# Performance work log

Measured on AMD Instinct MI355X. Metric: run time of the kernel, lower is better.

The kernel has to match this reference:

```python
import jax, jax.numpy as jnp
import numpy as np

K = 20  # neighbors


def knn_idx(x, k):
    # x: [B, C, N]; returns indices of k nearest neighbors (incl. self): [B, N, k]
    xx = jnp.sum(x * x, axis=1)                          # [B, N]
    inner = jnp.einsum('bcn,bcm->bnm', x, x)             # [B, N, N]
    pd = 2.0 * inner - xx[:, :, None] - xx[:, None, :]   # -squared distance
    _, idx = jax.lax.top_k(pd, k)                        # [B, N, k]
    return idx


def graph_feature(x, k):
    # x: [B, C, N] -> edge features [B, 2C, N, k]
    idx = knn_idx(x, k)                                  # [B, N, k]
    xt = jnp.swapaxes(x, 1, 2)                           # [B, N, C]
    nbr = jax.vmap(lambda f, i: f[i])(xt, idx)           # [B, N, k, C]
    ctr = xt[:, :, None, :]                              # [B, N, 1, C]
    feat = jnp.concatenate(
        [nbr - ctr, jnp.broadcast_to(ctr, nbr.shape)], axis=-1)  # [B, N, k, 2C]
    return jnp.transpose(feat, (0, 3, 1, 2))             # [B, 2C, N, k]


def blk2(x, w, s, t):
    # 1x1 Conv2d (no bias) + folded BN + LeakyReLU(0.2); x: [B, C, N, k]
    y = jnp.einsum('oc,bcnk->bonk', w, x)
    y = y * s[None, :, None, None] + t[None, :, None, None]
    return jax.nn.leaky_relu(y, 0.2)


def blk1(x, w, s, t):
    # 1x1 Conv1d (no bias) + folded BN + LeakyReLU(0.2); x: [B, C, N]
    y = jnp.einsum('oc,bcn->bon', w, x)
    y = y * s[None, :, None] + t[None, :, None]
    return jax.nn.leaky_relu(y, 0.2)


def setup_inputs() -> dict:
    key = jax.random.key(0)
    ks = jax.random.split(key, 32)
    inp = {'x': jax.random.normal(ks[0], (16, 2, 2048), jnp.float32)}
    wdims = [(64, 4), (64, 64), (64, 128), (64, 64), (64, 128),
             (1024, 192), (512, 1216), (256, 512), (1, 256)]
    for i, (o, c) in enumerate(wdims):
        inp[f'w{i+1}'] = jax.random.normal(ks[1 + i], (o, c), jnp.float32) * np.float32((2.0 / c) ** 0.5)
    bdims = [64, 64, 64, 64, 64, 1024, 512, 256]
    for i, d in enumerate(bdims):
        inp[f's{i+1}'] = jax.random.uniform(ks[10 + i], (d,), jnp.float32, 0.5, 1.5)
        inp[f't{i+1}'] = jax.random.normal(ks[18 + i], (d,), jnp.float32) * 0.1
    return inp


def reference(x, w1, w2, w3, w4, w5, w6, w7, w8, w9,
              s1, s2, s3, s4, s5, s6, s7, s8,
              t1, t2, t3, t4, t5, t6, t7, t8):
    B, _, N = x.shape
    h = graph_feature(x, K)                 # [B, 4, N, k]
    h = blk2(h, w1, s1, t1)
    h = blk2(h, w2, s2, t2)
    x1 = jnp.max(h, axis=-1)                # [B, 64, N]
    h = graph_feature(x1, K)                # [B, 128, N, k]
    h = blk2(h, w3, s3, t3)
    h = blk2(h, w4, s4, t4)
    x2 = jnp.max(h, axis=-1)                # [B, 64, N]
    h = graph_feature(x2, K)                # [B, 128, N, k]
    h = blk2(h, w5, s5, t5)
    x3 = jnp.max(h, axis=-1)                # [B, 64, N]
    cat = jnp.concatenate([x1, x2, x3], axis=1)   # [B, 192, N]
    e = blk1(cat, w6, s6, t6)               # [B, 1024, N]
    g = jnp.max(e, axis=-1, keepdims=True)  # global max [B, 1024, 1]
    g = jnp.broadcast_to(g, (B, g.shape[1], N))
    h = jnp.concatenate([g, x1, x2, x3], axis=1)  # [B, 1216, N]
    h = blk1(h, w7, s7, t7)
    h = blk1(h, w8, s8, t8)                 # dropout = identity (eval)
    y = jnp.einsum('oc,bcn->bon', w9, h)    # [B, 1, N]
    return jax.nn.sigmoid(y.reshape(B, -1))
```

## Files before the change

kernel.cpp:

```cpp
#include <hip/hip_runtime.h>
#include <math.h>

#define KNNK 20
#define BEFORE(v1, g1, v2, g2) (((v1) > (v2)) || ((v1) == (v2) && (g1) < (g2)))

typedef unsigned short u16;
typedef unsigned int u32;
typedef unsigned long long u64;
typedef __attribute__((ext_vector_type(8))) short short8v;
typedef __attribute__((ext_vector_type(4))) float f32x4;

__device__ __forceinline__ float lrelu(float v) { return v >= 0.f ? v : 0.2f * v; }

__device__ __forceinline__ u16 f2bf(float v) {
    u32 u = __float_as_uint(v);
    u += 0x7fffu + ((u >> 16) & 1u);
    return (u16)(u >> 16);
}
__device__ __forceinline__ float bf2f(u16 h) { return __uint_as_float(((u32)h) << 16); }

__device__ __forceinline__ u32 ordf(float v) {
    u32 u = __float_as_uint(v);
    return u ^ ((u32)((int)u >> 31) | 0x80000000u);
}
__device__ __forceinline__ u64 mkkey(float v, int g) {
    return ((u64)ordf(v) << 32) | (u32)(~(u32)g);
}

__device__ __forceinline__ void cvt8(const float* __restrict__ p, short8v& H8, short8v& M8, short8v& L8) {
    float4 a = *(const float4*)(p);
    float4 b4 = *(const float4*)(p + 4);
    float v[8] = {a.x, a.y, a.z, a.w, b4.x, b4.y, b4.z, b4.w};
    short8v H, M, L;
#pragma unroll
    for (int i = 0; i < 8; ++i) {
        float x = v[i];
        u16 h = f2bf(x);
        float r1 = x - bf2f(h);
        u16 m = f2bf(r1);
        float r2 = r1 - bf2f(m);
        H[i] = (short)h;
        M[i] = (short)m;
        L[i] = (short)f2bf(r2);
    }
    H8 = H; M8 = M; L8 = L;
}

__global__ __launch_bounds__(256) void xx_kernel(const float* __restrict__ f, long bstride, int C,
                                                 float* __restrict__ xx) {
    int i = blockIdx.x * 256 + threadIdx.x;
    int b = i >> 11, n = i & 2047;
    const float* fb = f + (long)b * bstride;
    float s = 0.f;
    for (int c = 0; c < C; ++c) { float v = fb[c * 2048 + n]; s = fmaf(v, v, s); }
    xx[i] = s;
}

__device__ __forceinline__ void topk_row(const float* __restrict__ srow, int lane, int* __restrict__ orow) {
    float b1 = -INFINITY, b2 = -INFINITY, b3 = -INFINITY;
    int j1 = 0, j2 = 0, j3 = 0;
#pragma unroll
    for (int j = 0; j < 32; ++j) {
        float vv = srow[lane + 64 * j];
        bool c1 = vv > b1;
        bool c2 = vv > b2;
        bool c3 = vv > b3;
        b3 = c2 ? b2 : (c3 ? vv : b3);
        j3 = c2 ? j2 : (c3 ? j : j3);
        b2 = c1 ? b1 : (c2 ? vv : b2);
        j2 = c1 ? j1 : (c2 ? j : j2);
        b1 = c1 ? vv : b1;
        j1 = c1 ? j : j1;
    }
    u64 ka = mkkey(b1, lane + (j1 << 6));
#pragma unroll
    for (int size = 2; size <= 64; size <<= 1) {
#pragma unroll
        for (int stride = size >> 1; stride >= 1; stride >>= 1) {
            u64 ok = __shfl_xor(ka, stride);
            bool low = (lane & stride) == 0;
            bool asc = (lane & size) == 0;
            bool f = ka > ok;
            bool take = (low == asc) ? f : !f;
            ka = take ? ka : ok;
        }
    }
    u64 w19 = __shfl(ka, 19);
    unsigned used = (1u << j1) | (1u << j2) | (1u << j3);
    u64 pend = mkkey(b2, lane + (j2 << 6));
    int pstate = 0;
    while (__any(pend > w19)) {
        u64 act = __ballot(pend > w19);
        int L = __ffsll((long long)act) - 1;
        u64 ck = __shfl(pend, L);
        u64 cfb = __ballot(lane < 20 && ck > ka);
        int p = 20 - __popcll(cfb);
        u64 up = __shfl_up(ka, 1);
        if (lane < 20) {
            if (lane > p) ka = up;
            else if (lane == p) ka = ck;
        }
        if (lane == L) {
            if (pstate == 0) {
                pend = mkkey(b3, lane + (j3 << 6));
                pstate = 1;
            } else {
                float nb = -INFINITY;
                int nj = 0;
#pragma unroll
                for (int j = 0; j < 32; ++j) {
                    float vvv = ((used >> j) & 1u) ? -INFINITY : srow[lane + 64 * j];
                    if (vvv > nb) { nb = vvv; nj = j; }
                }
                used |= 1u << nj;
                pend = mkkey(nb, lane + (nj << 6));
            }
        }
        w19 = __shfl(ka, 19);
    }
    if (lane < KNNK) orow[lane] = (int)(~(u32)ka) & 2047;
}

__device__ __forceinline__ u64 topk20_half(const float* __restrict__ srow, int lane, int colbase) {
    float b1 = -INFINITY, b2 = -INFINITY, b3 = -INFINITY;
    int j1 = 0, j2 = 0, j3 = 0;
#pragma unroll
    for (int j = 0; j < 16; ++j) {
        float vv = srow[lane + 64 * j];
        bool c1 = vv > b1;
        bool c2 = vv > b2;
        bool c3 = vv > b3;
        b3 = c2 ? b2 : (c3 ? vv : b3);
        j3 = c2 ? j2 : (c3 ? j : j3);
        b2 = c1 ? b1 : (c2 ? vv : b2);
        j2 = c1 ? j1 : (c2 ? j : j2);
        b1 = c1 ? vv : b1;
        j1 = c1 ? j : j1;
    }
    u64 ka = mkkey(b1, colbase + lane + (j1 << 6));
#pragma unroll
    for (int size = 2; size <= 64; size <<= 1) {
#pragma unroll
        for (int stride = size >> 1; stride >= 1; stride >>= 1) {
            u64 ok = __shfl_xor(ka, stride);
            bool low = (lane & stride) == 0;
            bool asc = (lane & size) == 0;
            bool f = ka > ok;
            bool take = (low == asc) ? f : !f;
            ka = take ? ka : ok;
        }
    }
    u64 w19 = __shfl(ka, 19);
    unsigned used = (1u << j1) | (1u << j2) | (1u << j3);
    u64 pend = mkkey(b2, colbase + lane + (j2 << 6));
    int pstate = 0;
    while (__any(pend > w19)) {
        u64 act = __ballot(pend > w19);
        int L = __ffsll((long long)act) - 1;
        u64 ck = __shfl(pend, L);
        u64 cfb = __ballot(lane < 20 && ck > ka);
        int p = 20 - __popcll(cfb);
        u64 up = __shfl_up(ka, 1);
        if (lane < 20) {
            if (lane > p) ka = up;
            else if (lane == p) ka = ck;
        }
        if (lane == L) {
            if (pstate == 0) {
                pend = mkkey(b3, colbase + lane + (j3 << 6));
                pstate = 1;
            } else {
                float nb = -INFINITY;
                int nj = 0;
#pragma unroll
                for (int j = 0; j < 16; ++j) {
                    float vvv = ((used >> j) & 1u) ? -INFINITY : srow[lane + 64 * j];
                    if (vvv > nb) { nb = vvv; nj = j; }
                }
                used |= 1u << nj;
                pend = mkkey(nb, colbase + lane + (nj << 6));
            }
        }
        w19 = __shfl(ka, 19);
    }
    return ka;
}

__device__ __forceinline__ u64 merge20(u64 kA, u64 kB, int lane) {
    u64 kb = __shfl(kB, (lane - 20) & 63);
    u64 ka = lane < 20 ? kA : (lane < 40 ? kb : 0ULL);
#pragma unroll
    for (int size = 2; size <= 64; size <<= 1) {
#pragma unroll
        for (int stride = size >> 1; stride >= 1; stride >>= 1) {
            u64 ok = __shfl_xor(ka, stride);
            bool low = (lane & stride) == 0;
            bool asc = (lane & size) == 0;
            bool f = ka > ok;
            bool take = (low == asc) ? f : !f;
            ka = take ? ka : ok;
        }
    }
    return ka;
}

__global__ __launch_bounds__(512, 4) void knn_kernel(const float* __restrict__ f, long bstride, int C,
                                                     const float* __restrict__ xx, int* __restrict__ idx_out) {
    __shared__ __align__(16) float pd[8 * 2048];
    __shared__ __align__(16) float Asm[16 * 64];
    int b = blockIdx.y;
    int n0 = blockIdx.x * 16;
    int t = threadIdx.x;
    const float* fb = f + (long)b * bstride;

    for (int e = t; e < C * 16; e += 512) {
        int c = e >> 4, j = e & 15;
        Asm[e] = fb[c * 2048 + n0 + j];
    }
    __syncthreads();

    float acc[16][4];
#pragma unroll
    for (int i = 0; i < 16; ++i)
#pragma unroll
        for (int j = 0; j < 4; ++j) acc[i][j] = 0.f;
    int m0 = t * 4;
    for (int c = 0; c < C; ++c) {
        float4 b4 = *(const float4*)(fb + c * 2048 + m0);
        float bv[4] = {b4.x, b4.y, b4.z, b4.w};
        const float* ar = Asm + c * 16;
        float4 a0 = *(const float4*)(ar);
        float4 a1 = *(const float4*)(ar + 4);
        float4 a2 = *(const float4*)(ar + 8);
        float4 a3 = *(const float4*)(ar + 12);
        float av[16] = {a0.x, a0.y, a0.z, a0.w, a1.x, a1.y, a1.z, a1.w,
                        a2.x, a2.y, a2.z, a2.w, a3.x, a3.y, a3.z, a3.w};
#pragma unroll
        for (int i = 0; i < 16; ++i)
#pragma unroll
            for (int j = 0; j < 4; ++j) acc[i][j] = fmaf(av[i], bv[j], acc[i][j]);
    }
    float4 xm4 = *(const float4*)(xx + b * 2048 + m0);
    float xm[4] = {xm4.x, xm4.y, xm4.z, xm4.w};

    int wave = t >> 6, lane = t & 63;

    {
        float4 xa0 = *(const float4*)(xx + b * 2048 + n0);
        float4 xa1 = *(const float4*)(xx + b * 2048 + n0 + 4);
        float xn[8] = {xa0.x, xa0.y, xa0.z, xa0.w, xa1.x, xa1.y, xa1.z, xa1.w};
#pragma unroll
        for (int i = 0; i < 8; ++i) {
            float4 o;
            o.x = (2.f * acc[i][0] - xn[i]) - xm[0];
            o.y = (2.f * acc[i][1] - xn[i]) - xm[1];
            o.z = (2.f * acc[i][2] - xn[i]) - xm[2];
            o.w = (2.f * acc[i][3] - xn[i]) - xm[3];
            *(float4*)(pd + i * 2048 + m0) = o;
        }
    }
    __syncthreads();
    topk_row(pd + wave * 2048, lane, idx_out + ((long)b * 2048 + n0 + wave) * KNNK);
    __syncthreads();

    {
        float4 xb0 = *(const float4*)(xx + b * 2048 + n0 + 8);
        float4 xb1 = *(const float4*)(xx + b * 2048 + n0 + 12);
        float xn[8] = {xb0.x, xb0.y, xb0.z, xb0.w, xb1.x, xb1.y, xb1.z, xb1.w};
#pragma unroll
        for (int i = 0; i < 8; ++i) {
            float4 o;
            o.x = (2.f * acc[8 + i][0] - xn[i]) - xm[0];
            o.y = (2.f * acc[8 + i][1] - xn[i]) - xm[1];
            o.z = (2.f * acc[8 + i][2] - xn[i]) - xm[2];
            o.w = (2.f * acc[8 + i][3] - xn[i]) - xm[3];
            *(float4*)(pd + i * 2048 + m0) = o;
        }
    }
    __syncthreads();
    topk_row(pd + wave * 2048, lane, idx_out + ((long)b * 2048 + n0 + 8 + wave) * KNNK);
}

__global__ __launch_bounds__(256) void split3t_kernel(const float* __restrict__ src, long bstride,
                                                      u16* __restrict__ oh, u16* __restrict__ om,
                                                      u16* __restrict__ ol) {
    __shared__ float lds[32][65];
    int b = blockIdx.y;
    int kt = blockIdx.x & 1, nt = blockIdx.x >> 1;
    int k0 = kt * 32, n0 = nt * 64, t = threadIdx.x;
#pragma unroll
    for (int i = 0; i < 8; ++i) {
        int e = t + i * 256;
        int k = e >> 6, n = e & 63;
        lds[k][n] = src[(long)b * bstride + (long)(k0 + k) * 2048 + n0 + n];
    }
    __syncthreads();
    int n = t >> 2, kq = t & 3;
    u16 hv[8], mv[8], lv[8];
#pragma unroll
    for (int i = 0; i < 8; ++i) {
        float v = lds[kq * 8 + i][n];
        u16 h = f2bf(v);
        float r1 = v - bf2f(h);
        u16 m = f2bf(r1);
        float r2 = r1 - bf2f(m);
        hv[i] = h; mv[i] = m; lv[i] = f2bf(r2);
    }
    long off = ((long)b * 2048 + n0 + n) * 64 + k0 + kq * 8;
    uint4 uh, um, ul;
    uh.x = (u32)hv[0] | ((u32)hv[1] << 16); uh.y = (u32)hv[2] | ((u32)hv[3] << 16);
    uh.z = (u32)hv[4] | ((u32)hv[5] << 16); uh.w = (u32)hv[6] | ((u32)hv[7] << 16);
    um.x = (u32)mv[0] | ((u32)mv[1] << 16); um.y = (u32)mv[2] | ((u32)mv[3] << 16);
    um.z = (u32)mv[4] | ((u32)mv[5] << 16); um.w = (u32)mv[6] | ((u32)mv[7] << 16);
    ul.x = (u32)lv[0] | ((u32)lv[1] << 16); ul.y = (u32)lv[2] | ((u32)lv[3] << 16);
    ul.z = (u32)lv[4] | ((u32)lv[5] << 16); ul.w = (u32)lv[6] | ((u32)lv[7] << 16);
    *(uint4*)(oh + off) = uh;
    *(uint4*)(om + off) = um;
    *(uint4*)(ol + off) = ul;
}

__global__ __launch_bounds__(512, 4) void knn_mfma_kernel(const u16* __restrict__ Sh, const u16* __restrict__ Sm,
                                                          const u16* __restrict__ Sl, const float* __restrict__ xx,
                                                          int* __restrict__ idx_out) {
    __shared__ __align__(16) float pd[16 * 1028];
    int b = blockIdx.y, n0 = blockIdx.x * 16, t = threadIdx.x;
    int wave = t >> 6, lane = t & 63, l15 = lane & 15, lq = lane >> 4;
    const u16* bh_ = Sh + (long)b * 2048 * 64;
    const u16* bm_ = Sm + (long)b * 2048 * 64;
    const u16* bl_ = Sl + (long)b * 2048 * 64;

    long ab = (long)(n0 + l15) * 64 + lq * 8;
    short8v ah0 = *(const short8v*)(bh_ + ab), ah1 = *(const short8v*)(bh_ + ab + 32);
    short8v am0 = *(const short8v*)(bm_ + ab), am1 = *(const short8v*)(bm_ + ab + 32);
    short8v al0 = *(const short8v*)(bl_ + ab), al1 = *(const short8v*)(bl_ + ab + 32);
    float4 xn4 = *(const float4*)(xx + b * 2048 + n0 + lq * 4);
    float xn[4] = {xn4.x, xn4.y, xn4.z, xn4.w};

    u64 kA0 = 0, kA1 = 0, kB0 = 0, kB1 = 0;
#pragma unroll
    for (int half = 0; half < 2; ++half) {
        int jb = half * 1024 + wave * 128;
        short8v Bh0[2], Bh1[2], Bm0[2], Bm1[2], Bl0[2], Bl1[2];
        {
            long bb = (long)(jb + l15) * 64 + lq * 8;
            Bh0[0] = *(const short8v*)(bh_ + bb); Bh1[0] = *(const short8v*)(bh_ + bb + 32);
            Bm0[0] = *(const short8v*)(bm_ + bb); Bm1[0] = *(const short8v*)(bm_ + bb + 32);
            Bl0[0] = *(const short8v*)(bl_ + bb); Bl1[0] = *(const short8v*)(bl_ + bb + 32);
        }
#pragma unroll
        for (int tt = 0; tt < 8; ++tt) {
            const int cur = tt & 1, nxt = cur ^ 1;
            if (tt < 7) {
                long bb = (long)(jb + (tt + 1) * 16 + l15) * 64 + lq * 8;
                Bh0[nxt] = *(const short8v*)(bh_ + bb); Bh1[nxt] = *(const short8v*)(bh_ + bb + 32);
                Bm0[nxt] = *(const short8v*)(bm_ + bb); Bm1[nxt] = *(const short8v*)(bm_ + bb + 32);
                Bl0[nxt] = *(const short8v*)(bl_ + bb); Bl1[nxt] = *(const short8v*)(bl_ + bb + 32);
            }
            f32x4 p = {0.f, 0.f, 0.f, 0.f}, q = {0.f, 0.f, 0.f, 0.f};
            p = __builtin_amdgcn_mfma_f32_16x16x32_bf16(ah0, Bh0[cur], p, 0, 0, 0);
            q = __builtin_amdgcn_mfma_f32_16x16x32_bf16(ah0, Bm0[cur], q, 0, 0, 0);
            p = __builtin_amdgcn_mfma_f32_16x16x32_bf16(am0, Bh0[cur], p, 0, 0, 0);
            q = __builtin_amdgcn_mfma_f32_16x16x32_bf16(am0, Bm0[cur], q, 0, 0, 0);
            p = __builtin_amdgcn_mfma_f32_16x16x32_bf16(ah0, Bl0[cur], p, 0, 0, 0);
            q = __builtin_amdgcn_mfma_f32_16x16x32_bf16(al0, Bh0[cur], q, 0, 0, 0);
            p = __builtin_amdgcn_mfma_f32_16x16x32_bf16(ah1, Bh1[cur], p, 0, 0, 0);
            q = __builtin_amdgcn_mfma_f32_16x16x32_bf16(ah1, Bm1[cur], q, 0, 0, 0);
            p = __builtin_amdgcn_mfma_f32_16x16x32_bf16(am1, Bh1[cur], p, 0, 0, 0);
            q = __builtin_amdgcn_mfma_f32_16x16x32_bf16(am1, Bm1[cur], q, 0, 0, 0);
            p = __builtin_amdgcn_mfma_f32_16x16x32_bf16(ah1, Bl1[cur], p, 0, 0, 0);
            q = __builtin_amdgcn_mfma_f32_16x16x32_bf16(al1, Bh1[cur], q, 0, 0, 0);
            int col = jb + tt * 16 + l15;
            float xmc = xx[(long)b * 2048 + col];
            f32x4 r = p + q;
            int lcol = col - half * 1024;
            pd[(lq * 4 + 0) * 1028 + lcol] = (2.f * r[0] - xn[0]) - xmc;
            pd[(lq * 4 + 1) * 1028 + lcol] = (2.f * r[1] - xn[1]) - xmc;
            pd[(lq * 4 + 2) * 1028 + lcol] = (2.f * r[2] - xn[2]) - xmc;
            pd[(lq * 4 + 3) * 1028 + lcol] = (2.f * r[3] - xn[3]) - xmc;
        }
        __syncthreads();
        if (half == 0) {
            kA0 = topk20_half(pd + (2 * wave) * 1028, lane, 0);
            kA1 = topk20_half(pd + (2 * wave + 1) * 1028, lane, 0);
            __syncthreads();
        } else {
            kB0 = topk20_half(pd + (2 * wave) * 1028, lane, 1024);
            kB1 = topk20_half(pd + (2 * wave + 1) * 1028, lane, 1024);
        }
    }
    u64 f0 = merge20(kA0, kB0, lane);
    u64 f1 = merge20(kA1, kB1, lane);
    if (lane < KNNK) {
        idx_out[((long)b * 2048 + n0 + 2 * wave) * KNNK + lane] = (int)(~(u32)f0) & 2047;
        idx_out[((long)b * 2048 + n0 + 2 * wave + 1) * KNNK + lane] = (int)(~(u32)f1) & 2047;
    }
}

__global__ __launch_bounds__(256) void pq_kernel(const float* __restrict__ f, long bstride, int C,
                                                 const float* __restrict__ W, float* __restrict__ P,
                                                 float* __restrict__ Q) {
    __shared__ __align__(16) float wa[64 * 64];
    __shared__ __align__(16) float wq[64 * 64];
    __shared__ __align__(16) float X[64 * 64];
    int b = blockIdx.y, n0 = blockIdx.x * 64, t = threadIdx.x;
    const float* fb = f + (long)b * bstride;
    for (int e = t; e < C * 64; e += 256) {
        int k = e >> 6, c = e & 63;
        float a = W[c * 2 * C + k];
        float bv = W[c * 2 * C + C + k];
        wa[k * 64 + c] = a;
        wq[k * 64 + c] = bv - a;
    }
    for (int e = t; e < C * 64; e += 256) {
        int k = e >> 6, j = e & 63;
        X[e] = fb[k * 2048 + n0 + j];
    }
    __syncthreads();
    int cg = t >> 4, ng = t & 15;
    float accP[4][4] = {}, accQ[4][4] = {};
    for (int k = 0; k < C; ++k) {
        float4 a4 = *(const float4*)(wa + k * 64 + cg * 4);
        float4 q4 = *(const float4*)(wq + k * 64 + cg * 4);
        float4 x4 = *(const float4*)(X + k * 64 + ng * 4);
        float av[4] = {a4.x, a4.y, a4.z, a4.w};
        float qv[4] = {q4.x, q4.y, q4.z, q4.w};
        float xv[4] = {x4.x, x4.y, x4.z, x4.w};
#pragma unroll
        for (int i = 0; i < 4; ++i)
#pragma unroll
            for (int j = 0; j < 4; ++j) {
                accP[i][j] = fmaf(av[i], xv[j], accP[i][j]);
                accQ[i][j] = fmaf(qv[i], xv[j], accQ[i][j]);
            }
    }
#pragma unroll
    for (int j = 0; j < 4; ++j) {
        long n = n0 + ng * 4 + j;
        float4 pv = {accP[0][j], accP[1][j], accP[2][j], accP[3][j]};
        float4 qv = {accQ[0][j], accQ[1][j], accQ[2][j], accQ[3][j]};
        *(float4*)(P + ((long)b * 2048 + n) * 64 + cg * 4) = pv;
        *(float4*)(Q + ((long)b * 2048 + n) * 64 + cg * 4) = qv;
    }
}

__global__ __launch_bounds__(256) void splitw3_kernel(const float* __restrict__ W, u16* __restrict__ h,
                                                      u16* __restrict__ m, u16* __restrict__ l) {
    int i = blockIdx.x * 256 + threadIdx.x;
    float v = W[i];
    u16 hh = f2bf(v);
    float r1 = v - bf2f(hh);
    u16 mm = f2bf(r1);
    float r2 = r1 - bf2f(mm);
    h[i] = hh;
    m[i] = mm;
    l[i] = f2bf(r2);
}

__global__ __launch_bounds__(256) void edge2_mfma_kernel(
    const float* __restrict__ P, const float* __restrict__ Q, const int* __restrict__ idx,
    const u16* __restrict__ Wh, const u16* __restrict__ Wm, const u16* __restrict__ Wl,
    const float* __restrict__ sa, const float* __restrict__ ta, const float* __restrict__ sb,
    const float* __restrict__ tb, float* __restrict__ out, int cofs) {
    __shared__ __align__(16) float h1t[192 * 68];
    __shared__ int idxl[160];
    int b = blockIdx.y, n0 = blockIdx.x * 8, t = threadIdx.x;
    if (t < 160) idxl[t] = idx[((long)b * 2048 + n0) * KNNK + t];
    __syncthreads();

    for (int it = t; it < 2560; it += 256) {
        int col = it % 160, cg = it / 160;
        int p = col / 20;
        int j = idxl[col];
        int n = n0 + p;
        float4 pv = *(const float4*)(P + ((long)b * 2048 + j) * 64 + cg * 4);
        float4 qv = *(const float4*)(Q + ((long)b * 2048 + n) * 64 + cg * 4);
        float4 sv = *(const float4*)(sa + cg * 4);
        float4 tv = *(const float4*)(ta + cg * 4);
        float4 o;
        o.x = lrelu(fmaf(sv.x, pv.x + qv.x, tv.x));
        o.y = lrelu(fmaf(sv.y, pv.y + qv.y, tv.y));
        o.z = lrelu(fmaf(sv.z, pv.z + qv.z, tv.z));
        o.w = lrelu(fmaf(sv.w, pv.w + qv.w, tv.w));
        *(float4*)(h1t + col * 68 + cg * 4) = o;
    }
    for (int it = t; it < 512; it += 256) {
        int col = 160 + (it & 31), cg = it >> 5;
        float4 z = {0.f, 0.f, 0.f, 0.f};
        *(float4*)(h1t + col * 68 + cg * 4) = z;
    }
    __syncthreads();

    int wave = t >> 6, lane = t & 63, l15 = lane & 15, lq = lane >> 4;
    f32x4 acc[3][4];
#pragma unroll
    for (int ct = 0; ct < 3; ++ct)
#pragma unroll
        for (int mt = 0; mt < 4; ++mt) {
            f32x4 z = {0.f, 0.f, 0.f, 0.f};
            acc[ct][mt] = z;
        }

#pragma unroll
    for (int ct = 0; ct < 3; ++ct) {
        int col = (wave * 3 + ct) * 16 + l15;
        short8v bh[2], bm[2], bl[2];
#pragma unroll
        for (int kh = 0; kh < 2; ++kh) cvt8(h1t + col * 68 + kh * 32 + lq * 8, bh[kh], bm[kh], bl[kh]);
#pragma unroll
        for (int mt = 0; mt < 4; ++mt) {
#pragma unroll
            for (int kh = 0; kh < 2; ++kh) {
                int wo = (mt * 16 + l15) * 64 + kh * 32 + lq * 8;
                short8v ah = *(const short8v*)(Wh + wo);
                short8v am = *(const short8v*)(Wm + wo);
                short8v al = *(const short8v*)(Wl + wo);
                acc[ct][mt] = __builtin_amdgcn_mfma_f32_16x16x32_bf16(ah, bh[kh], acc[ct][mt], 0, 0, 0);
                acc[ct][mt] = __builtin_amdgcn_mfma_f32_16x16x32_bf16(ah, bm[kh], acc[ct][mt], 0, 0, 0);
                acc[ct][mt] = __builtin_amdgcn_mfma_f32_16x16x32_bf16(am, bh[kh], acc[ct][mt], 0, 0, 0);
                acc[ct][mt] = __builtin_amdgcn_mfma_f32_16x16x32_bf16(am, bm[kh], acc[ct][mt], 0, 0, 0);
                acc[ct][mt] = __builtin_amdgcn_mfma_f32_16x16x32_bf16(ah, bl[kh], acc[ct][mt], 0, 0, 0);
                acc[ct][mt] = __builtin_amdgcn_mfma_f32_16x16x32_bf16(al, bh[kh], acc[ct][mt], 0, 0, 0);
            }
        }
    }
    __syncthreads();

#pragma unroll
    for (int ct = 0; ct < 3; ++ct) {
        int col = (wave * 3 + ct) * 16 + l15;
#pragma unroll
        for (int mt = 0; mt < 4; ++mt) {
            float4 d = {acc[ct][mt][0], acc[ct][mt][1], acc[ct][mt][2], acc[ct][mt][3]};
            *(float4*)(h1t + col * 68 + mt * 16 + lq * 4) = d;
        }
    }
    __syncthreads();

    for (int id = t; id < 512; id += 256) {
        int co = id & 63, p = id >> 6;
        float sv = sb[co], tv = tb[co];
        float m = -INFINITY;
#pragma unroll 4
        for (int kk = 0; kk < KNNK; ++kk)
            m = fmaxf(m, lrelu(fmaf(sv, h1t[(p * 20 + kk) * 68 + co], tv)));
        out[(long)b * (192 * 2048) + (long)(cofs + co) * 2048 + n0 + p] = m;
    }
}

__global__ __launch_bounds__(256) void edge2_kernel(
    const float* __restrict__ P, const float* __restrict__ Q, const int* __restrict__ idx,
    const float* __restrict__ W2, const float* __restrict__ sa, const float* __restrict__ ta,
    const float* __restrict__ sb, const float* __restrict__ tb, float* __restrict__ out, int cofs) {
    __shared__ __align__(16) float h1[64 * 164];
    __shared__ __align__(16) float w2l[64 * 64];
    __shared__ int idxl[160];
    int b = blockIdx.y, n0 = blockIdx.x * 8, t = threadIdx.x;
    if (t < 160) idxl[t] = idx[((long)b * 2048 + n0) * KNNK + t];
    for (int e = t; e < 4096; e += 256) { int co = e >> 6, ci = e & 63; w2l[ci * 64 + co] = W2[e]; }
    __syncthreads();
    for (int it = t; it < 2560; it += 256) {
        int col = it % 160, cg = it / 160;
        int p = col / 20;
        int j = idxl[col];
        int n = n0 + p;
        float4 pv = *(const float4*)(P + ((long)b * 2048 + j) * 64 + cg * 4);
        float4 qv = *(const float4*)(Q + ((long)b * 2048 + n) * 64 + cg * 4);
        float4 sv = *(const float4*)(sa + cg * 4);
        float4 tv = *(const float4*)(ta + cg * 4);
        h1[(cg * 4 + 0) * 164 + col] = lrelu(fmaf(sv.x, pv.x + qv.x, tv.x));
        h1[(cg * 4 + 1) * 164 + col] = lrelu(fmaf(sv.y, pv.y + qv.y, tv.y));
        h1[(cg * 4 + 2) * 164 + col] = lrelu(fmaf(sv.z, pv.z + qv.z, tv.z));
        h1[(cg * 4 + 3) * 164 + col] = lrelu(fmaf(sv.w, pv.w + qv.w, tv.w));
    }
    __syncthreads();
    int p = t & 7, co2 = t >> 3, c0 = co2 * 2;
    float acc0[20], acc1[20];
#pragma unroll
    for (int q = 0; q < 20; ++q) { acc0[q] = 0.f; acc1[q] = 0.f; }
#pragma unroll 4
    for (int k = 0; k < 64; ++k) {
        float2 w = *(const float2*)(w2l + k * 64 + c0);
        const float* hr = h1 + k * 164 + p * 20;
#pragma unroll
        for (int q = 0; q < 5; ++q) {
            float4 h4 = *(const float4*)(hr + q * 4);
            acc0[q * 4 + 0] = fmaf(w.x, h4.x, acc0[q * 4 + 0]);
            acc0[q * 4 + 1] = fmaf(w.x, h4.y, acc0[q * 4 + 1]);
            acc0[q * 4 + 2] = fmaf(w.x, h4.z, acc0[q * 4 + 2]);
            acc0[q * 4 + 3] = fmaf(w.x, h4.w, acc0[q * 4 + 3]);
            acc1[q * 4 + 0] = fmaf(w.y, h4.x, acc1[q * 4 + 0]);
            acc1[q * 4 + 1] = fmaf(w.y, h4.y, acc1[q * 4 + 1]);
            acc1[q * 4 + 2] = fmaf(w.y, h4.z, acc1[q * 4 + 2]);
            acc1[q * 4 + 3] = fmaf(w.y, h4.w, acc1[q * 4 + 3]);
        }
    }
    float s0 = sb[c0], t0v = tb[c0], s1 = sb[c0 + 1], t1v = tb[c0 + 1];
    float m0 = -INFINITY, m1 = -INFINITY;
#pragma unroll
    for (int q = 0; q < 20; ++q) {
        m0 = fmaxf(m0, lrelu(fmaf(s0, acc0[q], t0v)));
        m1 = fmaxf(m1, lrelu(fmaf(s1, acc1[q], t1v)));
    }
    out[(long)b * (192 * 2048) + (long)(cofs + c0) * 2048 + n0 + p] = m0;
    out[(long)b * (192 * 2048) + (long)(cofs + c0 + 1) * 2048 + n0 + p] = m1;
}

__global__ __launch_bounds__(256) void edge1_kernel(const float* __restrict__ P, const float* __restrict__ Q,
                                                    const int* __restrict__ idx, const float* __restrict__ s,
                                                    const float* __restrict__ tt, float* __restrict__ out,
                                                    int cofs) {
    __shared__ int idxl[80];
    int b = blockIdx.y, n0 = blockIdx.x * 4, t = threadIdx.x;
    int c = t & 63, p = t >> 6;
    if (t < 80) idxl[t] = idx[((long)b * 2048 + n0) * KNNK + t];
    __syncthreads();
    float qv = Q[((long)b * 2048 + n0 + p) * 64 + c];
    float sc = s[c], tc = tt[c];
    float m = -INFINITY;
    for (int kk = 0; kk < KNNK; ++kk) {
        int j = idxl[p * KNNK + kk];
        float v = P[((long)b * 2048 + j) * 64 + c];
        m = fmaxf(m, lrelu(fmaf(sc, v + qv, tc)));
    }
    out[(long)b * (192 * 2048) + (long)(cofs + c) * 2048 + n0 + p] = m;
}

__global__ __launch_bounds__(256) void gemm_kernel(
    const float* __restrict__ W, int ldw, int Kdim, const float* __restrict__ X, long xbstride,
    const float* __restrict__ s, const float* __restrict__ tvec, const float* __restrict__ bias, int M,
    float* __restrict__ out, long obstride, float* __restrict__ maxout) {
    __shared__ __align__(16) float wl[32 * 68];
    __shared__ __align__(16) float xl[32 * 132];
    int b = blockIdx.z, ct = blockIdx.x * 64, nt = blockIdx.y * 128, t = threadIdx.x;
    const float* Xb = X + (long)b * xbstride;
    int cg = t >> 4, ng = t & 15;
    float acc[4][8];
#pragma unroll
    for (int i = 0; i < 4; ++i)
#pragma unroll
        for (int j = 0; j < 8; ++j) acc[i][j] = 0.f;
    for (int k0 = 0; k0 < Kdim; k0 += 32) {
        __syncthreads();
        for (int e = t; e < 2048; e += 256) {
            int c = e >> 5, k = e & 31;
            wl[k * 68 + c] = W[(long)(ct + c) * ldw + k0 + k];
        }
        for (int e = t; e < 4096; e += 256) {
            int k = e >> 7, j = e & 127;
            xl[k * 132 + j] = Xb[(long)(k0 + k) * 2048 + nt + j];
        }
        __syncthreads();
#pragma unroll 8
        for (int k = 0; k < 32; ++k) {
            float4 w4 = *(const float4*)(wl + k * 68 + cg * 4);
            float4 xa = *(const float4*)(xl + k * 132 + ng * 4);
            float4 xb = *(const float4*)(xl + k * 132 + 64 + ng * 4);
            float wv[4] = {w4.x, w4.y, w4.z, w4.w};
            float xv[8] = {xa.x, xa.y, xa.z, xa.w, xb.x, xb.y, xb.z, xb.w};
#pragma unroll
            for (int i = 0; i < 4; ++i)
#pragma unroll
                for (int j = 0; j < 8; ++j) acc[i][j] = fmaf(wv[i], xv[j], acc[i][j]);
        }
    }
    if (maxout) {
        __syncthreads();
        float* scr = xl;
#pragma unroll
        for (int i = 0; i < 4; ++i) {
            int c = ct + cg * 4 + i;
            float sv = s[c], tv = tvec[c];
            float m = -INFINITY;
#pragma unroll
            for (int j = 0; j < 8; ++j) m = fmaxf(m, lrelu(fmaf(sv, acc[i][j], tv)));
            scr[(cg * 4 + i) * 16 + ng] = m;
        }
        __syncthreads();
        if (t < 64) {
            float m = scr[t * 16];
            for (int j = 1; j < 16; ++j) m = fmaxf(m, scr[t * 16 + j]);
            maxout[((long)b * M + ct + t) * 16 + blockIdx.y] = m;
        }
    } else {
#pragma unroll
        for (int i = 0; i < 4; ++i) {
            int c = ct + cg * 4 + i;
            float bv = bias ? bias[b * M + c] : 0.f;
            float sv = s[c], tv = tvec[c];
            float4 o0, o1;
            o0.x = lrelu(fmaf(sv, acc[i][0] + bv, tv));
            o0.y = lrelu(fmaf(sv, acc[i][1] + bv, tv));
            o0.z = lrelu(fmaf(sv, acc[i][2] + bv, tv));
            o0.w = lrelu(fmaf(sv, acc[i][3] + bv, tv));
            o1.x = lrelu(fmaf(sv, acc[i][4] + bv, tv));
            o1.y = lrelu(fmaf(sv, acc[i][5] + bv, tv));
            o1.z = lrelu(fmaf(sv, acc[i][6] + bv, tv));
            o1.w = lrelu(fmaf(sv, acc[i][7] + bv, tv));
            float* op = out + (long)b * obstride + (long)c * 2048 + nt + ng * 4;
            *(float4*)op = o0;
            *(float4*)(op + 64) = o1;
        }
    }
}

__global__ __launch_bounds__(256) void splitw_kernel(const float* __restrict__ W, int ldw, int koff, int K,
                                                     long total, u16* __restrict__ hi, u16* __restrict__ lo) {
    long i = (long)blockIdx.x * 256 + threadIdx.x;
    if (i >= total) return;
    long m = i / K, k = i - m * K;
    float v = W[m * ldw + koff + k];
    u16 h = f2bf(v);
    hi[i] = h;
    lo[i] = f2bf(v - bf2f(h));
}

__global__ __launch_bounds__(256) void splitx_kernel(const float* __restrict__ cat, u16* __restrict__ hi,
                                                     u16* __restrict__ lo) {
    __shared__ float lds[32][65];
    int b = blockIdx.y;
    int kt = blockIdx.x % 6, nt = blockIdx.x / 6;
    int k0 = kt * 32, n0 = nt * 64;
    int t = threadIdx.x;
#pragma unroll
    for (int i = 0; i < 8; ++i) {
        int e = t + i * 256;
        int k = e >> 6, n = e & 63;
        lds[k][n] = cat[(long)b * (192 * 2048) + (long)(k0 + k) * 2048 + n0 + n];
    }
    __syncthreads();
    int n = t >> 2, kq = t & 3;
    u16 hv[8], lv[8];
#pragma unroll
    for (int i = 0; i < 8; ++i) {
        float v = lds[kq * 8 + i][n];
        u16 h = f2bf(v);
        hv[i] = h;
        lv[i] = f2bf(v - bf2f(h));
    }
    long off = ((long)b * 2048 + n0 + n) * 192 + k0 + kq * 8;
    uint4 uh, ul;
    uh.x = (u32)hv[0] | ((u32)hv[1] << 16); uh.y = (u32)hv[2] | ((u32)hv[3] << 16);
    uh.z = (u32)hv[4] | ((u32)hv[5] << 16); uh.w = (u32)hv[6] | ((u32)hv[7] << 16);
    ul.x = (u32)lv[0] | ((u32)lv[1] << 16); ul.y = (u32)lv[2] | ((u32)lv[3] << 16);
    ul.z = (u32)lv[4] | ((u32)lv[5] << 16); ul.w = (u32)lv[6] | ((u32)lv[7] << 16);
    *(uint4*)(hi + off) = uh;
    *(uint4*)(lo + off) = ul;
}

template <int MT, int NT, bool MAXOUT>
__global__ __launch_bounds__(256, 2) void gemm_mfma(
    const u16* __restrict__ Whi, const u16* __restrict__ Wlo, const u16* __restrict__ Xhi,
    const u16* __restrict__ Xlo, int K, int M, const float* __restrict__ s,
    const float* __restrict__ tvec, const float* __restrict__ bias, float* __restrict__ outf,
    long obstride, u16* __restrict__ ohi, u16* __restrict__ olo, int oK, float* __restrict__ maxout) {
    constexpr int BM = MT * 32, BN = NT * 32;
    __shared__ __align__(16) u16 Ah[BM * 32], Al[BM * 32], Bh[BN * 32], Bl[BN * 32];
    __shared__ float scr[MAXOUT ? BM * 2 : 1];

    int b = blockIdx.z;
    int m0 = blockIdx.x * BM;
    int n0 = blockIdx.y * BN;
    int t = threadIdx.x;
    int wave = t >> 6, lane = t & 63;
    int wm = (wave >> 1) * (MT * 16);
    int wn = (wave & 1) * (NT * 16);
    const int l15 = lane & 15, lq = lane >> 4;
    const int kcs = lq ^ ((l15 >> 1) & 3);

    const u16* Xbh = Xhi + (long)b * 2048 * K;
    const u16* Xbl = Xlo + (long)b * 2048 * K;

    f32x4 zero4 = {0.f, 0.f, 0.f, 0.f};
    f32x4 acc[MT][NT];
#pragma unroll
    for (int i = 0; i < MT; ++i)
#pragma unroll
        for (int j = 0; j < NT; ++j) acc[i][j] = zero4;

    for (int k0 = 0; k0 < K; k0 += 32) {
        __syncthreads();
#pragma unroll
        for (int u = t; u < BM * 4; u += 256) {
            int row = u >> 2, kc = (u & 3) ^ ((row >> 1) & 3);
            long ga = (long)(m0 + row) * K + k0 + kc * 8;
            *(uint4*)(Ah + u * 8) = *(const uint4*)(Whi + ga);
            *(uint4*)(Al + u * 8) = *(const uint4*)(Wlo + ga);
        }
#pragma unroll
        for (int u = t; u < BN * 4; u += 256) {
            int row = u >> 2, kc = (u & 3) ^ ((row >> 1) & 3);
            long ga = (long)(n0 + row) * K + k0 + kc * 8;
            *(uint4*)(Bh + u * 8) = *(const uint4*)(Xbh + ga);
            *(uint4*)(Bl + u * 8) = *(const uint4*)(Xbl + ga);
        }
        __syncthreads();
        short8v a_h[MT], a_l[MT], b_h[NT], b_l[NT];
#pragma unroll
        for (int i = 0; i < MT; ++i) {
            int u = (wm + i * 16 + l15) * 4 + kcs;
            a_h[i] = *(const short8v*)(Ah + u * 8);
            a_l[i] = *(const short8v*)(Al + u * 8);
        }
#pragma unroll
        for (int j = 0; j < NT; ++j) {
            int u = (wn + j * 16 + l15) * 4 + kcs;
            b_h[j] = *(const short8v*)(Bh + u * 8);
            b_l[j] = *(const short8v*)(Bl + u * 8);
        }
#pragma unroll
        for (int i = 0; i < MT; ++i)
#pragma unroll
            for (int j = 0; j < NT; ++j) {
                acc[i][j] = __builtin_amdgcn_mfma_f32_16x16x32_bf16(a_h[i], b_h[j], acc[i][j], 0, 0, 0);
                acc[i][j] = __builtin_amdgcn_mfma_f32_16x16x32_bf16(a_h[i], b_l[j], acc[i][j], 0, 0, 0);
                acc[i][j] = __builtin_amdgcn_mfma_f32_16x16x32_bf16(a_l[i], b_h[j], acc[i][j], 0, 0, 0);
            }
    }

    if constexpr (MAXOUT) {
#pragma unroll
        for (int i = 0; i < MT; ++i)
#pragma unroll
            for (int r = 0; r < 4; ++r) {
                int ml = wm + i * 16 + lq * 4 + r;
                int c = m0 + ml;
                float sv = s[c], tv = tvec[c];
                float mx = -INFINITY;
#pragma unroll
                for (int j = 0; j < NT; ++j) mx = fmaxf(mx, lrelu(fmaf(sv, acc[i][j][r], tv)));
                mx = fmaxf(mx, __shfl_xor(mx, 1));
                mx = fmaxf(mx, __shfl_xor(mx, 2));
                mx = fmaxf(mx, __shfl_xor(mx, 4));
                mx = fmaxf(mx, __shfl_xor(mx, 8));
                if (l15 == 0) scr[ml * 2 + (wave & 1)] = mx;
            }
        __syncthreads();
        if (t < BM) maxout[((long)b * M + m0 + t) * 16 + blockIdx.y] = fmaxf(scr[t * 2], scr[t * 2 + 1]);
    } else if (outf) {
#pragma unroll
        for (int i = 0; i < MT; ++i)
#pragma unroll
            for (int r = 0; r < 4; ++r) {
                int c = m0 + wm + i * 16 + lq * 4 + r;
                float sv = s[c], tv = tvec[c];
                float bv = bias ? bias[b * M + c] : 0.f;
                float* op = outf + (long)b * obstride + (long)c * 2048 + n0 + wn;
#pragma unroll
                for (int j = 0; j < NT; ++j) op[j * 16 + l15] = lrelu(fmaf(sv, acc[i][j][r] + bv, tv));
            }
    } else {
#pragma unroll
        for (int i = 0; i < MT; ++i) {
            float sv[4], tv[4], bv[4];
#pragma unroll
            for (int r = 0; r < 4; ++r) {
                int c = m0 + wm + i * 16 + lq * 4 + r;
                sv[r] = s[c];
                tv[r] = tvec[c];
                bv[r] = bias ? bias[b * M + c] : 0.f;
            }
#pragma unroll
            for (int j = 0; j < NT; ++j) {
                long nb = ((long)b * 2048 + n0 + wn + j * 16 + l15) * oK + m0 + wm + i * 16 + lq * 4;
                ushort4 uh, ul;
                float v0 = lrelu(fmaf(sv[0], acc[i][j][0] + bv[0], tv[0]));
                float v1 = lrelu(fmaf(sv[1], acc[i][j][1] + bv[1], tv[1]));
                float v2 = lrelu(fmaf(sv[2], acc[i][j][2] + bv[2], tv[2]));
                float v3 = lrelu(fmaf(sv[3], acc[i][j][3] + bv[3], tv[3]));
                u16 h0 = f2bf(v0), h1 = f2bf(v1), h2 = f2bf(v2), h3 = f2bf(v3);
                uh.x = h0; uh.y = h1; uh.z = h2; uh.w = h3;
                ul.x = f2bf(v0 - bf2f(h0));
                ul.y = f2bf(v1 - bf2f(h1));
                ul.z = f2bf(v2 - bf2f(h2));
                ul.w = f2bf(v3 - bf2f(h3));
                *(ushort4*)(ohi + nb) = uh;
                *(ushort4*)(olo + nb) = ul;
            }
        }
    }
}

__global__ __launch_bounds__(256) void gmax_final(const float* __restrict__ ep, float* __restrict__ g) {
    int i = blockIdx.x * 256 + threadIdx.x;
    float m = ep[i * 16];
    for (int j = 1; j < 16; ++j) m = fmaxf(m, ep[i * 16 + j]);
    g[i] = m;
}

__global__ __launch_bounds__(64) void bias7_kernel(const float* __restrict__ w7, const float* __restrict__ g,
                                                   float* __restrict__ bias7) {
    int o = blockIdx.x;
    int b = o >> 9, co = o & 511;
    int lane = threadIdx.x;
    float acc = 0.f;
    for (int j = lane; j < 1024; j += 64) acc = fmaf(w7[(long)co * 1216 + j], g[b * 1024 + j], acc);
#pragma unroll
    for (int off = 32; off >= 1; off >>= 1) acc += __shfl_xor(acc, off);
    if (lane == 0) bias7[o] = acc;
}

__global__ __launch_bounds__(256) void w9_kernel(const float* __restrict__ w9, const float* __restrict__ h8,
                                                 float* __restrict__ out) {
    int i = blockIdx.x * 256 + threadIdx.x;
    int b = i >> 11, n = i & 2047;
    const float* hb = h8 + (long)b * 256 * 2048 + n;
    float acc = 0.f;
    for (int c = 0; c < 256; ++c) acc = fmaf(w9[c], hb[c * 2048], acc);
    out[i] = 1.f / (1.f + expf(-acc));
}

extern "C" void kernel_launch(void* const* d_in, const int* in_sizes, int n_in,
                              void* d_out, int out_size, void* d_ws, size_t ws_size,
                              hipStream_t stream) {
    (void)in_sizes; (void)n_in; (void)out_size;
    const float* x  = (const float*)d_in[0];
    const float* w1 = (const float*)d_in[1];
    const float* w2 = (const float*)d_in[2];
    const float* w3 = (const float*)d_in[3];
    const float* w4 = (const float*)d_in[4];
    const float* w5 = (const float*)d_in[5];
    const float* w6 = (const float*)d_in[6];
    const float* w7 = (const float*)d_in[7];
    const float* w8 = (const float*)d_in[8];
    const float* w9 = (const float*)d_in[9];
    const float* s1 = (const float*)d_in[10]; const float* t1 = (const float*)d_in[11];
    const float* s2 = (const float*)d_in[12]; const float* t2 = (const float*)d_in[13];
    const float* s3 = (const float*)d_in[14]; const float* t3 = (const float*)d_in[15];
    const float* s4 = (const float*)d_in[16]; const float* t4 = (const float*)d_in[17];
    const float* s5 = (const float*)d_in[18]; const float* t5 = (const float*)d_in[19];
    const float* s6 = (const float*)d_in[20]; const float* t6 = (const float*)d_in[21];
    const float* s7 = (const float*)d_in[22]; const float* t7 = (const float*)d_in[23];
    const float* s8 = (const float*)d_in[24]; const float* t8 = (const float*)d_in[25];

    float* cat = (float*)d_ws;
    float* xxb = cat + (long)6291456;
    int* idxb = (int*)(xxb + 32768);
    float* ep = (float*)(idxb + 655360);
    float* g  = ep + 262144;
    float* b7 = g + 16384;
    float* h8 = b7 + 8192;
    float* P  = h8 + 8388608;
    float* Q  = P + 2097152;
    u16* h7hi = (u16*)(Q + 2097152);
    u16* h7lo = h7hi + 16777216;
    u16* cathi = h7lo + 16777216;
    u16* catlo = cathi + 6291456;
    u16* w6h = catlo + 6291456;
    u16* w6l = w6h + 196608;
    u16* w7h = w6l + 196608;
    u16* w7l = w7h + 98304;
    u16* w8h = w7l + 98304;
    u16* w8l = w8h + 131072;
    const size_t NEED = 173375488;
    bool big = ws_size >= NEED;

    u16* w2L = h7hi;
    u16* w4L = h7hi + 12288;
    u16* Sh = h7hi + 32768;
    u16* Sm = Sh + 2097152;
    u16* Sl = Sm + 2097152;

    dim3 blk(256);
    dim3 blk512(512);
    long catstride = 192 * 2048;

    if (big) {
        splitw3_kernel<<<16, blk, 0, stream>>>(w2, w2L, w2L + 4096, w2L + 8192);
        splitw3_kernel<<<16, blk, 0, stream>>>(w4, w4L, w4L + 4096, w4L + 8192);
    }

    xx_kernel<<<128, blk, 0, stream>>>(x, 2 * 2048, 2, xxb);
    knn_kernel<<<dim3(128, 16), blk512, 0, stream>>>(x, 2 * 2048, 2, xxb, idxb);
    pq_kernel<<<dim3(32, 16), blk, 0, stream>>>(x, 2 * 2048, 2, w1, P, Q);
    if (big)
        edge2_mfma_kernel<<<dim3(256, 16), blk, 0, stream>>>(P, Q, idxb, w2L, w2L + 4096, w2L + 8192,
                                                             s1, t1, s2, t2, cat, 0);
    else
        edge2_kernel<<<dim3(256, 16), blk, 0, stream>>>(P, Q, idxb, w2, s1, t1, s2, t2, cat, 0);
    xx_kernel<<<128, blk, 0, stream>>>(cat, catstride, 64, xxb);
    if (big) {
        split3t_kernel<<<dim3(64, 16), blk, 0, stream>>>(cat, catstride, Sh, Sm, Sl);
        knn_mfma_kernel<<<dim3(128, 16), blk512, 0, stream>>>(Sh, Sm, Sl, xxb, idxb);
    } else {
        knn_kernel<<<dim3(128, 16), blk512, 0, stream>>>(cat, catstride, 64, xxb, idxb);
    }
    pq_kernel<<<dim3(32, 16), blk, 0, stream>>>(cat, catstride, 64, w3, P, Q);
    if (big)
        edge2_mfma_kernel<<<dim3(256, 16), blk, 0, stream>>>(P, Q, idxb, w4L, w4L + 4096, w4L + 8192,
                                                             s3, t3, s4, t4, cat, 64);
    else
        edge2_kernel<<<dim3(256, 16), blk, 0, stream>>>(P, Q, idxb, w4, s3, t3, s4, t4, cat, 64);
    xx_kernel<<<128, blk, 0, stream>>>(cat + 64 * 2048, catstride, 64, xxb);
    if (big) {
        split3t_kernel<<<dim3(64, 16), blk, 0, stream>>>(cat + 64 * 2048, catstride, Sh, Sm, Sl);
        knn_mfma_kernel<<<dim3(128, 16), blk512, 0, stream>>>(Sh, Sm, Sl, xxb, idxb);
    } else {
        knn_kernel<<<dim3(128, 16), blk512, 0, stream>>>(cat + 64 * 2048, catstride, 64, xxb, idxb);
    }
    pq_kernel<<<dim3(32, 16), blk, 0, stream>>>(cat + 64 * 2048, catstride, 64, w5, P, Q);
    edge1_kernel<<<dim3(512, 16), blk, 0, stream>>>(P, Q, idxb, s5, t5, cat, 128);

    if (big) {
        splitw_kernel<<<768, blk, 0, stream>>>(w6, 192, 0, 192, 196608, w6h, w6l);
        splitw_kernel<<<384, blk, 0, stream>>>(w7, 1216, 1024, 192, 98304, w7h, w7l);
        splitw_kernel<<<512, blk, 0, stream>>>(w8, 512, 0, 512, 131072, w8h, w8l);
        splitx_kernel<<<dim3(192, 16), blk, 0, stream>>>(cat, cathi, catlo);
        gemm_mfma<4, 4, true><<<dim3(8, 16, 16), blk, 0, stream>>>(
            w6h, w6l, cathi, catlo, 192, 1024, s6, t6, nullptr, nullptr, 0, nullptr, nullptr, 0, ep);
        gmax_final<<<64, blk, 0, stream>>>(ep, g);
        bias7_kernel<<<dim3(16 * 512), dim3(64), 0, stream>>>(w7, g, b7);
        gemm_mfma<4, 4, false><<<dim3(4, 16, 16), blk, 0, stream>>>(
            w7h, w7l, cathi, catlo, 192, 512, s7, t7, b7, nullptr, 0, h7hi, h7lo, 512, nullptr);
        gemm_mfma<2, 4, false><<<dim3(4, 16, 16), blk, 0, stream>>>(
            w8h, w8l, h7hi, h7lo, 512, 256, s8, t8, nullptr, h8, (long)256 * 2048, nullptr, nullptr, 0,
            nullptr);
        w9_kernel<<<128, blk, 0, stream>>>(w9, h8, (float*)d_out);
    } else {
        float* h7f = (float*)h7hi;
        gemm_kernel<<<dim3(16, 16, 16), blk, 0, stream>>>(w6, 192, 192, cat, catstride, s6, t6, nullptr,
                                                          1024, nullptr, 0, ep);
        gmax_final<<<64, blk, 0, stream>>>(ep, g);
        bias7_kernel<<<dim3(16 * 512), dim3(64), 0, stream>>>(w7, g, b7);
        gemm_kernel<<<dim3(8, 16, 16), blk, 0, stream>>>(w7 + 1024, 1216, 192, cat, catstride, s7, t7, b7,
                                                         512, h7f, (long)512 * 2048, nullptr);
        gemm_kernel<<<dim3(4, 16, 16), blk, 0, stream>>>(w8, 512, 512, h7f, (long)512 * 2048, s8, t8,
                                                         nullptr, 256, h8, (long)256 * 2048, nullptr);
        w9_kernel<<<128, blk, 0, stream>>>(w9, h8, (float*)d_out);
    }
}
```

Measured before the change: 1.192 ms.

## Split kNN distance work between MFMA waves and FP32 VALU waves

The kNN kernel now gives two waves the bf16x3 MFMA distance tiles for 640 columns per half. The other six waves compute the remaining 384 columns with plain FP32 FMAs, using a 16-point query tile staged in LDS. The aim is to run the matrix cores and vector ALUs at the same time rather than leaving the VALUs idle. The risk is load imbalance between the two groups, since each MFMA wave now handles 20 tiles. The half loop is also no longer unrolled.

```diff
diff --git a/kernel.cpp b/kernel.cpp
--- a/kernel.cpp
+++ b/kernel.cpp
@@ -2,7 +2,6 @@
 #include <math.h>
 
 #define KNNK 20
-#define BEFORE(v1, g1, v2, g2) (((v1) > (v2)) || ((v1) == (v2) && (g1) < (g2)))
 
 typedef unsigned short u16;
 typedef unsigned int u32;
@@ -319,64 +318,103 @@
     *(uint4*)(ol + off) = ul;
 }
 
-__global__ __launch_bounds__(512, 4) void knn_mfma_kernel(const u16* __restrict__ Sh, const u16* __restrict__ Sm,
-                                                          const u16* __restrict__ Sl, const float* __restrict__ xx,
-                                                          int* __restrict__ idx_out) {
+__global__ __launch_bounds__(512, 4) void knn_hybrid_kernel(
+    const float* __restrict__ f, long bstride, const u16* __restrict__ Sh, const u16* __restrict__ Sm,
+    const u16* __restrict__ Sl, const float* __restrict__ xx, int* __restrict__ idx_out) {
     __shared__ __align__(16) float pd[16 * 1028];
+    __shared__ __align__(16) float Asm[64 * 16];
     int b = blockIdx.y, n0 = blockIdx.x * 16, t = threadIdx.x;
     int wave = t >> 6, lane = t & 63, l15 = lane & 15, lq = lane >> 4;
+    const float* fb = f + (long)b * bstride;
     const u16* bh_ = Sh + (long)b * 2048 * 64;
     const u16* bm_ = Sm + (long)b * 2048 * 64;
     const u16* bl_ = Sl + (long)b * 2048 * 64;
 
-    long ab = (long)(n0 + l15) * 64 + lq * 8;
-    short8v ah0 = *(const short8v*)(bh_ + ab), ah1 = *(const short8v*)(bh_ + ab + 32);
-    short8v am0 = *(const short8v*)(bm_ + ab), am1 = *(const short8v*)(bm_ + ab + 32);
-    short8v al0 = *(const short8v*)(bl_ + ab), al1 = *(const short8v*)(bl_ + ab + 32);
-    float4 xn4 = *(const float4*)(xx + b * 2048 + n0 + lq * 4);
-    float xn[4] = {xn4.x, xn4.y, xn4.z, xn4.w};
+    for (int e = t; e < 64 * 16; e += 512) {
+        int c = e >> 4, j = e & 15;
+        Asm[e] = fb[c * 2048 + n0 + j];
+    }
+
+    short8v ah0 = {}, ah1 = {}, am0 = {}, am1 = {}, al0 = {}, al1 = {};
+    float xnm[4] = {0.f, 0.f, 0.f, 0.f};
+    float xnv[16];
+    if (wave < 2) {
+        long ab = (long)(n0 + l15) * 64 + lq * 8;
+        ah0 = *(const short8v*)(bh_ + ab); ah1 = *(const short8v*)(bh_ + ab + 32);
+        am0 = *(const short8v*)(bm_ + ab); am1 = *(const short8v*)(bm_ + ab + 32);
+        al0 = *(const short8v*)(bl_ + ab); al1 = *(const short8v*)(bl_ + ab + 32);
+        float4 xn4 = *(const float4*)(xx + b * 2048 + n0 + lq * 4);
+        xnm[0] = xn4.x; xnm[1] = xn4.y; xnm[2] = xn4.z; xnm[3] = xn4.w;
+    } else {
+#pragma unroll
+        for (int i = 0; i < 16; ++i) xnv[i] = xx[b * 2048 + n0 + i];
+    }
+    __syncthreads();
 
     u64 kA0 = 0, kA1 = 0, kB0 = 0, kB1 = 0;
-#pragma unroll
+#pragma unroll 1
     for (int half = 0; half < 2; ++half) {
-        int jb = half * 1024 + wave * 128;
-        short8v Bh0[2], Bh1[2], Bm0[2], Bm1[2], Bl0[2], Bl1[2];
-        {
-            long bb = (long)(jb + l15) * 64 + lq * 8;
-            Bh0[0] = *(const short8v*)(bh_ + bb); Bh1[0] = *(const short8v*)(bh_ + bb + 32);
-            Bm0[0] = *(const short8v*)(bm_ + bb); Bm1[0] = *(const short8v*)(bm_ + bb + 32);
-            Bl0[0] = *(const short8v*)(bl_ + bb); Bl1[0] = *(const short8v*)(bl_ + bb + 32);
-        }
-#pragma unroll
-        for (int tt = 0; tt < 8; ++tt) {
-            const int cur = tt & 1, nxt = cur ^ 1;
-            if (tt < 7) {
-                long bb = (long)(jb + (tt + 1) * 16 + l15) * 64 + lq * 8;
-                Bh0[nxt] = *(const short8v*)(bh_ + bb); Bh1[nxt] = *(const short8v*)(bh_ + bb + 32);
-                Bm0[nxt] = *(const short8v*)(bm_ + bb); Bm1[nxt] = *(const short8v*)(bm_ + bb + 32);
-                Bl0[nxt] = *(const short8v*)(bl_ + bb); Bl1[nxt] = *(const short8v*)(bl_ + bb + 32);
-            }
-            f32x4 p = {0.f, 0.f, 0.f, 0.f}, q = {0.f, 0.f, 0.f, 0.f};
-            p = __builtin_amdgcn_mfma_f32_16x16x32_bf16(ah0, Bh0[cur], p, 0, 0, 0);
-            q = __builtin_amdgcn_mfma_f32_16x16x32_bf16(ah0, Bm0[cur], q, 0, 0, 0);
-            p = __builtin_amdgcn_mfma_f32_16x16x32_bf16(am0, Bh0[cur], p, 0, 0, 0);
-            q = __builtin_amdgcn_mfma_f32_16x16x32_bf16(am0, Bm0[cur], q, 0, 0, 0);
-            p = __builtin_amdgcn_mfma_f32_16x16x32_bf16(ah0, Bl0[cur], p, 0, 0, 0);
-            q = __builtin_amdgcn_mfma_f32_16x16x32_bf16(al0, Bh0[cur], q, 0, 0, 0);
-            p = __builtin_amdgcn_mfma_f32_16x16x32_bf16(ah1, Bh1[cur], p, 0, 0, 0);
-            q = __builtin_amdgcn_mfma_f32_16x16x32_bf16(ah1, Bm1[cur], q, 0, 0, 0);
-            p = __builtin_amdgcn_mfma_f32_16x16x32_bf16(am1, Bh1[cur], p, 0, 0, 0);
-            q = __builtin_amdgcn_mfma_f32_16x16x32_bf16(am1, Bm1[cur], q, 0, 0, 0);
-            p = __builtin_amdgcn_mfma_f32_16x16x32_bf16(ah1, Bl1[cur], p, 0, 0, 0);
-            q = __builtin_amdgcn_mfma_f32_16x16x32_bf16(al1, Bh1[cur], q, 0, 0, 0);
-            int col = jb + tt * 16 + l15;
+        if (wave < 2) {
+            int jb = half * 1024 + wave * 320;
+            short8v Bh0[2], Bh1[2], Bm0[2], Bm1[2], Bl0[2], Bl1[2];
+            {
+                long bb = (long)(jb + l15) * 64 + lq * 8;
+                Bh0[0] = *(const short8v*)(bh_ + bb); Bh1[0] = *(const short8v*)(bh_ + bb + 32);
+                Bm0[0] = *(const short8v*)(bm_ + bb); Bm1[0] = *(const short8v*)(bm_ + bb + 32);
+                Bl0[0] = *(const short8v*)(bl_ + bb); Bl1[0] = *(const short8v*)(bl_ + bb + 32);
+            }
+#pragma unroll 2
+            for (int tt = 0; tt < 20; ++tt) {
+                const int cur = tt & 1, nxt = cur ^ 1;
+                if (tt < 19) {
+                    long bb = (long)(jb + (tt + 1) * 16 + l15) * 64 + lq * 8;
+                    Bh0[nxt] = *(const short8v*)(bh_ + bb); Bh1[nxt] = *(const short8v*)(bh_ + bb + 32);
+                    Bm0[nxt] = *(const short8v*)(bm_ + bb); Bm1[nxt] = *(const short8v*)(bm_ + bb + 32);
+                    Bl0[nxt] = *(const short8v*)(bl_ + bb); Bl1[nxt] = *(const short8v*)(bl_ + bb + 32);
+                }
+                f32x4 p = {0.f, 0.f, 0.f, 0.f}, q = {0.f, 0.f, 0.f, 0.f};
+                p = __builtin_amdgcn_mfma_f32_16x16x32_bf16(ah0, Bh0[cur], p, 0, 0, 0);
+                q = __builtin_amdgcn_mfma_f32_16x16x32_bf16(ah0, Bm0[cur], q, 0, 0, 0);
+                p = __builtin_amdgcn_mfma_f32_16x16x32_bf16(am0, Bh0[cur], p, 0, 0, 0);
+                q = __builtin_amdgcn_mfma_f32_16x16x32_bf16(am0, Bm0[cur], q, 0, 0, 0);
+                p = __builtin_amdgcn_mfma_f32_16x16x32_bf16(ah0, Bl0[cur], p, 0, 0, 0);
+                q = __builtin_amdgcn_mfma_f32_16x16x32_bf16(al0, Bh0[cur], q, 0, 0, 0);
+                p = __builtin_amdgcn_mfma_f32_16x16x32_bf16(ah1, Bh1[cur], p, 0, 0, 0);
+                q = __builtin_amdgcn_mfma_f32_16x16x32_bf16(ah1, Bm1[cur], q, 0, 0, 0);
+                p = __builtin_amdgcn_mfma_f32_16x16x32_bf16(am1, Bh1[cur], p, 0, 0, 0);
+                q = __builtin_amdgcn_mfma_f32_16x16x32_bf16(am1, Bm1[cur], q, 0, 0, 0);
+                p = __builtin_amdgcn_mfma_f32_16x16x32_bf16(ah1, Bl1[cur], p, 0, 0, 0);
+                q = __builtin_amdgcn_mfma_f32_16x16x32_bf16(al1, Bh1[cur], q, 0, 0, 0);
+                int col = jb + tt * 16 + l15;
+                float xmc = xx[(long)b * 2048 + col];
+                f32x4 r = p + q;
+                int lcol = col - half * 1024;
+                pd[(lq * 4 + 0) * 1028 + lcol] = (2.f * r[0] - xnm[0]) - xmc;
+                pd[(lq * 4 + 1) * 1028 + lcol] = (2.f * r[1] - xnm[1]) - xmc;
+                pd[(lq * 4 + 2) * 1028 + lcol] = (2.f * r[2] - xnm[2]) - xmc;
+                pd[(lq * 4 + 3) * 1028 + lcol] = (2.f * r[3] - xnm[3]) - xmc;
+            }
+        } else {
+            int col = half * 1024 + 640 + (wave - 2) * 64 + lane;
+            float acc[16];
+#pragma unroll
+            for (int i = 0; i < 16; ++i) acc[i] = 0.f;
+            for (int c = 0; c < 64; ++c) {
+                float bv = fb[c * 2048 + col];
+                const float* ar = Asm + c * 16;
+                float4 a0 = *(const float4*)(ar);
+                float4 a1 = *(const float4*)(ar + 4);
+                float4 a2 = *(const float4*)(ar + 8);
+                float4 a3 = *(const float4*)(ar + 12);
+                float av[16] = {a0.x, a0.y, a0.z, a0.w, a1.x, a1.y, a1.z, a1.w,
+                                a2.x, a2.y, a2.z, a2.w, a3.x, a3.y, a3.z, a3.w};
+#pragma unroll
+                for (int i = 0; i < 16; ++i) acc[i] = fmaf(av[i], bv, acc[i]);
+            }
             float xmc = xx[(long)b * 2048 + col];
-            f32x4 r = p + q;
             int lcol = col - half * 1024;
-            pd[(lq * 4 + 0) * 1028 + lcol] = (2.f * r[0] - xn[0]) - xmc;
-            pd[(lq * 4 + 1) * 1028 + lcol] = (2.f * r[1] - xn[1]) - xmc;
-            pd[(lq * 4 + 2) * 1028 + lcol] = (2.f * r[2] - xn[2]) - xmc;
-            pd[(lq * 4 + 3) * 1028 + lcol] = (2.f * r[3] - xn[3]) - xmc;
+#pragma unroll
+            for (int i = 0; i < 16; ++i) pd[i * 1028 + lcol] = (2.f * acc[i] - xnv[i]) - xmc;
         }
         __syncthreads();
         if (half == 0) {
@@ -980,7 +1018,7 @@
     xx_kernel<<<128, blk, 0, stream>>>(cat, catstride, 64, xxb);
     if (big) {
         split3t_kernel<<<dim3(64, 16), blk, 0, stream>>>(cat, catstride, Sh, Sm, Sl);
-        knn_mfma_kernel<<<dim3(128, 16), blk512, 0, stream>>>(Sh, Sm, Sl, xxb, idxb);
+        knn_hybrid_kernel<<<dim3(128, 16), blk512, 0, stream>>>(cat, catstride, Sh, Sm, Sl, xxb, idxb);
     } else {
         knn_kernel<<<dim3(128, 16), blk512, 0, stream>>>(cat, catstride, 64, xxb, idxb);
     }
@@ -993,7 +1031,8 @@
     xx_kernel<<<128, blk, 0, stream>>>(cat + 64 * 2048, catstride, 64, xxb);
     if (big) {
         split3t_kernel<<<dim3(64, 16), blk, 0, stream>>>(cat + 64 * 2048, catstride, Sh, Sm, Sl);
-        knn_mfma_kernel<<<dim3(128, 16), blk512, 0, stream>>>(Sh, Sm, Sl, xxb, idxb);
+        knn_hybrid_kernel<<<dim3(128, 16), blk512, 0, stream>>>(cat + 64 * 2048, catstride, Sh, Sm, Sl,
+                                                                xxb, idxb);
     } else {
         knn_kernel<<<dim3(128, 16), blk512, 0, stream>>>(cat + 64 * 2048, catstride, 64, xxb, idxb);
     }
```

Measured after the change: 1.287 ms. 8.0% more time.
